# Optimization experiments

Hardware: AMD Instinct MI355X
Metric: run time of the kernel (lower is better)

The kernel has to match this reference:

```python
import jax, jax.numpy as jnp
import numpy as np


def setup_inputs() -> dict:
    key = jax.random.key(0)
    kx, kq = jax.random.split(key)
    x = jax.random.normal(kx, (64, 1024, 1024), dtype=jnp.float32)
    # K=16 quantization points, sorted (the kernel assumes a fixed ordered set)
    qpoints = jnp.sort(jax.random.uniform(kq, (16,), dtype=jnp.float32,
                                          minval=-1.5, maxval=1.5))
    return {"x": x, "qpoints": qpoints}


def reference(x, qpoints):
    # Nearest-qpoint quantize without materializing an (N, K) distance matrix.
    # searchsorted gives, for each element, the index of the first qpoint >= x;
    # the nearest point is either that one or its left neighbor.
    K = qpoints.shape[0]
    idx = jnp.searchsorted(qpoints, x)            # in [0, K]
    lo = qpoints[jnp.clip(idx - 1, 0, K - 1)]     # left neighbor
    hi = qpoints[jnp.clip(idx, 0, K - 1)]         # right neighbor
    out = jnp.where(jnp.abs(x - lo) <= jnp.abs(x - hi), lo, hi)
    return out
```

## Files before the change

kernel.cpp:

```cpp
#include <hip/hip_runtime.h>


__device__ __forceinline__ float rfl(float v) {
    return __int_as_float(__builtin_amdgcn_readfirstlane(__float_as_int(v)));
}

__device__ __forceinline__ float quant1(float xv, const float qp[16]) {
    float hi = qp[15];
#pragma unroll
    for (int k = 14; k >= 0; --k) hi = (qp[k] >= xv) ? qp[k] : hi;
    float lo = qp[0];
#pragma unroll
    for (int k = 1; k < 16; ++k) lo = (qp[k] < xv) ? qp[k] : lo;
    return (fabsf(xv - lo) <= fabsf(xv - hi)) ? lo : hi;
}

__global__ __launch_bounds__(256) void qquant_vec4(
    const float4* __restrict__ x, const float* __restrict__ q,
    float4* __restrict__ out, int n4) {
    const float4* q4 = (const float4*)q;
    float4 q0 = q4[0], q1 = q4[1], q2 = q4[2], q3 = q4[3];
    float qp[16] = {rfl(q0.x), rfl(q0.y), rfl(q0.z), rfl(q0.w),
                    rfl(q1.x), rfl(q1.y), rfl(q1.z), rfl(q1.w),
                    rfl(q2.x), rfl(q2.y), rfl(q2.z), rfl(q2.w),
                    rfl(q3.x), rfl(q3.y), rfl(q3.z), rfl(q3.w)};

    int stride = gridDim.x * blockDim.x;
    for (int i = blockIdx.x * blockDim.x + threadIdx.x; i < n4; i += stride) {
        float4 v = x[i];
        float4 r;
        r.x = quant1(v.x, qp);
        r.y = quant1(v.y, qp);
        r.z = quant1(v.z, qp);
        r.w = quant1(v.w, qp);
        out[i] = r;
    }
}

__global__ void qquant_tail(const float* __restrict__ x,
                            const float* __restrict__ q,
                            float* __restrict__ out, int start, int n) {
    int i = start + threadIdx.x;
    if (i >= n) return;
    float qp[16];
#pragma unroll
    for (int k = 0; k < 16; ++k) qp[k] = q[k];
    out[i] = quant1(x[i], qp);
}

extern "C" void kernel_launch(void* const* d_in, const int* in_sizes, int n_in,
                              void* d_out, int out_size, void* d_ws, size_t ws_size,
                              hipStream_t stream) {
    const float* x = (const float*)d_in[0];
    const float* q = (const float*)d_in[1];
    float* out = (float*)d_out;
    int n = in_sizes[0];

    int n4 = n >> 2;
    if (n4 > 0) {
        int blocks = (n4 + 255) / 256;
        if (blocks > 8192) blocks = 8192;
        qquant_vec4<<<blocks, 256, 0, stream>>>((const float4*)x, q,
                                                (float4*)out, n4);
    }
    int rem = n & 3;
    if (rem > 0) {
        qquant_tail<<<1, 64, 0, stream>>>(x, q, out, n4 << 2, n);
    }
}
```

Before: 445.5 us.

## Add 8-way unrolled nontemporal kernel and single-pass bracket search

Adds a kernel in which each thread issues eight independent vector loads up front, striding by the grid, and uses nontemporal loads and stores. It runs when the element count divides evenly, which removes the grid-stride loop and raises memory-level parallelism. The quantizer now finds the lower and upper neighbours in one merged compare chain instead of two loops. The nontemporal hints and the larger per-thread register footprint may change occupancy and cache behaviour.

```diff
diff --git a/kernel.cpp b/kernel.cpp
--- a/kernel.cpp
+++ b/kernel.cpp
@@ -1,38 +1,71 @@
 #include <hip/hip_runtime.h>
 
 
-__device__ __forceinline__ float rfl(float v) {
-    return __int_as_float(__builtin_amdgcn_readfirstlane(__float_as_int(v)));
-}
+typedef float vfloat4 __attribute__((ext_vector_type(4)));
 
 __device__ __forceinline__ float quant1(float xv, const float qp[16]) {
-    float hi = qp[15];
+    bool c0 = qp[0] < xv;
+    float lo = qp[0];
+    float hi = c0 ? qp[1] : qp[0];
 #pragma unroll
-    for (int k = 14; k >= 0; --k) hi = (qp[k] >= xv) ? qp[k] : hi;
-    float lo = qp[0];
-#pragma unroll
-    for (int k = 1; k < 16; ++k) lo = (qp[k] < xv) ? qp[k] : lo;
+    for (int k = 1; k <= 14; ++k) {
+        bool c = qp[k] < xv;
+        lo = c ? qp[k] : lo;
+        hi = c ? qp[k + 1] : hi;
+    }
+    bool c15 = qp[15] < xv;
+    lo = c15 ? qp[15] : lo;
+    hi = c15 ? qp[15] : hi;
     return (fabsf(xv - lo) <= fabsf(xv - hi)) ? lo : hi;
 }
 
+__device__ __forceinline__ vfloat4 quant4(vfloat4 v, const float qp[16]) {
+    vfloat4 r;
+    r.x = quant1(v.x, qp);
+    r.y = quant1(v.y, qp);
+    r.z = quant1(v.z, qp);
+    r.w = quant1(v.w, qp);
+    return r;
+}
+
+__device__ __forceinline__ void load_qp(const float* __restrict__ q,
+                                        float qp[16]) {
+    const vfloat4* q4 = (const vfloat4*)q;
+    vfloat4 q0 = q4[0], q1 = q4[1], q2 = q4[2], q3 = q4[3];
+    qp[0] = q0.x; qp[1] = q0.y; qp[2] = q0.z; qp[3] = q0.w;
+    qp[4] = q1.x; qp[5] = q1.y; qp[6] = q1.z; qp[7] = q1.w;
+    qp[8] = q2.x; qp[9] = q2.y; qp[10] = q2.z; qp[11] = q2.w;
+    qp[12] = q3.x; qp[13] = q3.y; qp[14] = q3.z; qp[15] = q3.w;
+}
+
+__global__ __launch_bounds__(256) void qquant_x8(
+    const vfloat4* __restrict__ x, const float* __restrict__ q,
+    vfloat4* __restrict__ out) {
+    float qp[16];
+    load_qp(q, qp);
+
+    int stride = gridDim.x * 256;
+    int base = blockIdx.x * 256 + threadIdx.x;
+
+    vfloat4 v[8];
+#pragma unroll
+    for (int u = 0; u < 8; ++u)
+        v[u] = __builtin_nontemporal_load(&x[base + u * stride]);
+#pragma unroll
+    for (int u = 0; u < 8; ++u) {
+        vfloat4 r = quant4(v[u], qp);
+        __builtin_nontemporal_store(r, &out[base + u * stride]);
+    }
+}
+
 __global__ __launch_bounds__(256) void qquant_vec4(
-    const float4* __restrict__ x, const float* __restrict__ q,
-    float4* __restrict__ out, int n4) {
-    const float4* q4 = (const float4*)q;
-    float4 q0 = q4[0], q1 = q4[1], q2 = q4[2], q3 = q4[3];
-    float qp[16] = {rfl(q0.x), rfl(q0.y), rfl(q0.z), rfl(q0.w),
-                    rfl(q1.x), rfl(q1.y), rfl(q1.z), rfl(q1.w),
-                    rfl(q2.x), rfl(q2.y), rfl(q2.z), rfl(q2.w),
-                    rfl(q3.x), rfl(q3.y), rfl(q3.z), rfl(q3.w)};
-
+    const vfloat4* __restrict__ x, const float* __restrict__ q,
+    vfloat4* __restrict__ out, int n4) {
+    float qp[16];
+    load_qp(q, qp);
     int stride = gridDim.x * blockDim.x;
     for (int i = blockIdx.x * blockDim.x + threadIdx.x; i < n4; i += stride) {
-        float4 v = x[i];
-        float4 r;
-        r.x = quant1(v.x, qp);
-        r.y = quant1(v.y, qp);
-        r.z = quant1(v.z, qp);
-        r.w = quant1(v.w, qp);
+        vfloat4 r = quant4(x[i], qp);
         out[i] = r;
     }
 }
@@ -43,8 +76,7 @@
     int i = start + threadIdx.x;
     if (i >= n) return;
     float qp[16];
-#pragma unroll
-    for (int k = 0; k < 16; ++k) qp[k] = q[k];
+    load_qp(q, qp);
     out[i] = quant1(x[i], qp);
 }
 
@@ -57,11 +89,18 @@
     int n = in_sizes[0];
 
     int n4 = n >> 2;
+    const int ELEMS_PER_BLOCK = 256 * 8;
     if (n4 > 0) {
-        int blocks = (n4 + 255) / 256;
-        if (blocks > 8192) blocks = 8192;
-        qquant_vec4<<<blocks, 256, 0, stream>>>((const float4*)x, q,
-                                                (float4*)out, n4);
+        if (n4 % ELEMS_PER_BLOCK == 0) {
+            int blocks = n4 / ELEMS_PER_BLOCK;
+            qquant_x8<<<blocks, 256, 0, stream>>>((const vfloat4*)x, q,
+                                                  (vfloat4*)out);
+        } else {
+            int blocks = (n4 + 255) / 256;
+            if (blocks > 8192) blocks = 8192;
+            qquant_vec4<<<blocks, 256, 0, stream>>>((const vfloat4*)x, q,
+                                                    (vfloat4*)out, n4);
+        }
     }
     int rem = n & 3;
     if (rem > 0) {
```

Result: slower. 464.3 us (+4.2%).
